# Kernel tuning notes

Hardware: AMD Instinct MI355X
Metric: run time of the kernel (lower is better)

The kernel has to match this reference:

```python
import jax, jax.numpy as jnp
import numpy as np

K_RATIO = 0.2
EPS = 1e-6


def setup_inputs() -> dict:
    key = jax.random.key(0)
    k1, k2 = jax.random.split(key)
    B, C, D, H, W = 2, 4, 128, 128, 128
    logits = jax.random.normal(k1, (B, C, D, H, W), dtype=jnp.float32)
    labels = jax.random.randint(k2, (B, D, H, W), 0, C)
    # one-hot target along channel axis 1, matching the tensor-path `target` arg
    target = jax.nn.one_hot(labels, C, axis=1, dtype=jnp.float32)
    return {"logits": logits, "target": target}


def reference(logits, target):
    B, C = logits.shape[0], logits.shape[1]

    # ---- Top-K cross entropy (ignore_index=-1 -> all voxels valid) ----
    y = jnp.argmax(target, axis=1)  # [B, D, H, W] int labels
    logp = jax.nn.log_softmax(logits, axis=1)
    # CE per voxel: -logp[b, y, d, h, w]
    ce = -jnp.take_along_axis(logp, y[:, None], axis=1)[:, 0]  # [B, D, H, W]
    ce_flat = ce.reshape(B, -1)  # [B, N]
    N = ce_flat.shape[1]
    k = max(1, int(N * K_RATIO))  # static: all voxels valid, k < N
    topk_vals, _ = jax.lax.top_k(ce_flat, k)  # [B, k]
    topk_loss = jnp.mean(jnp.mean(topk_vals, axis=1))

    # ---- Soft dice (no valid_mask in tensor path) ----
    p = jax.nn.softmax(logits, axis=1)  # [B, C, D, H, W]
    spatial = tuple(range(2, p.ndim))
    num = 2.0 * jnp.sum(p * target, axis=spatial)          # [B, C]
    den = jnp.sum(p + target, axis=spatial) + EPS          # [B, C]
    dice = 1.0 - num / den                                  # [B, C]
    if C > 1:
        dice = dice[:, 1:]  # drop background channel
    dice_loss = jnp.mean(dice)

    return topk_loss + 0.5 * dice_loss
```

## Files before the change

### kernel.cpp

```cpp
#include <hip/hip_runtime.h>
#include <stdint.h>

#define NVOX (1u << 21)
#define NB   2
#define KSEL 419430u
#define TPB  256
#define VPB  4096
#define BPB  ((int)(NVOX / VPB))
#define NBLK (NB * BPB)
#define NITER ((int)(VPB / (TPB * 4)))
#define NCOPY 64
#define NHC  16
#define NBINS 4096
#define SH   19
#define FIXS 262144.0f

typedef unsigned long long ull;

__device__ __forceinline__ float wred64(float v) {
#pragma unroll
  for (int o = 32; o > 0; o >>= 1) v += __shfl_down(v, o, 64);
  return v;
}

__global__ __launch_bounds__(TPB, 4) void k1_fused(
    const float* __restrict__ logits, const float* __restrict__ target,
    ull* __restrict__ hist,
    float* __restrict__ dice_acc )
{
  __shared__ ull hbin[NBINS];
  const int tid = threadIdx.x;
  for (int i = tid; i < NBINS; i += TPB) hbin[i] = 0ull;
  __syncthreads();

  const int blk = blockIdx.x;
  const int b = blk / BPB;
  const size_t v0 = (size_t)(blk % BPB) * VPB;
  const float* lg = logits + (size_t)b * 4 * NVOX + v0;
  const float* tg = target + (size_t)b * 4 * NVOX + v0;

  float sp[4] = {0.f,0.f,0.f,0.f}, nm[4] = {0.f,0.f,0.f,0.f}, ct[4] = {0.f,0.f,0.f,0.f};

  float4 La[4], Ta[4], Lb[4], Tb[4];
#pragma unroll
  for (int c = 0; c < 4; ++c) {
    La[c] = *(const float4*)(lg + (size_t)c * NVOX + tid * 4);
    Ta[c] = *(const float4*)(tg + (size_t)c * NVOX + tid * 4);
  }

#pragma unroll
  for (int it = 0; it < NITER; ++it) {
    if (it + 1 < NITER) {
      const int inx = (it + 1) * (TPB * 4) + tid * 4;
#pragma unroll
      for (int c = 0; c < 4; ++c) {
        Lb[c] = *(const float4*)(lg + (size_t)c * NVOX + inx);
        Tb[c] = *(const float4*)(tg + (size_t)c * NVOX + inx);
      }
    }
#pragma unroll
    for (int j = 0; j < 4; ++j) {
      float l[4], t[4];
#pragma unroll
      for (int c = 0; c < 4; ++c) {
        l[c] = ((const float*)&La[c])[j];
        t[c] = ((const float*)&Ta[c])[j];
      }
      float m = fmaxf(fmaxf(l[0], l[1]), fmaxf(l[2], l[3]));
      float e[4]; float s = 0.f;
#pragma unroll
      for (int c = 0; c < 4; ++c) { e[c] = __expf(l[c] - m); s += e[c]; }
      float inv = 1.f / s;
      float lse = __logf(s);
      float ly = l[0]*t[0] + l[1]*t[1] + l[2]*t[2] + l[3]*t[3];
      float cev = (m - ly) + lse;
      uint32_t idx = __float_as_uint(cev) >> SH;
      if (idx > NBINS - 1) idx = NBINS - 1;
      ull pk = (1ull << 40) | (ull)(cev * FIXS);
      atomicAdd(&hbin[idx], pk);
#pragma unroll
      for (int c = 0; c < 4; ++c) {
        float p = e[c] * inv;
        sp[c] += p;
        nm[c] += p * t[c];
        ct[c] += t[c];
      }
    }
    if (it + 1 < NITER) {
#pragma unroll
      for (int c = 0; c < 4; ++c) { La[c] = Lb[c]; Ta[c] = Tb[c]; }
    }
  }

#pragma unroll
  for (int c = 0; c < 4; ++c) { sp[c] = wred64(sp[c]); nm[c] = wred64(nm[c]); ct[c] = wred64(ct[c]); }
  if ((tid & 63) == 0) {
    float* dst = dice_acc + ((size_t)(blk & (NCOPY - 1)) * NB + b) * 12;
#pragma unroll
    for (int c = 0; c < 4; ++c) {
      atomicAdd(dst + c,     sp[c]);
      atomicAdd(dst + 4 + c, nm[c]);
      atomicAdd(dst + 8 + c, ct[c]);
    }
  }
  __syncthreads();
  const size_t hoff = ((size_t)b * NHC + (size_t)(blk & (NHC - 1))) * NBINS;
  ull* hdst = hist + hoff;
  for (int i = tid; i < NBINS; i += TPB) {
    ull v = hbin[i];
    if (v) atomicAdd(&hdst[i], v);
  }
}

__global__ __launch_bounds__(256) void k_reduce(
    const ull* __restrict__ hist,
    uint32_t* __restrict__ rcnt, float* __restrict__ rsum)
{
  const int b = blockIdx.x >> 3;
  const int base = (blockIdx.x & 7) * 512 + threadIdx.x * 2;
  uint32_t c0 = 0, c1 = 0;
  ull s0 = 0, s1 = 0;
  for (int copy = 0; copy < NHC; ++copy) {
    const ull* src = hist + ((size_t)b * NHC + copy) * NBINS + base;
    ull v0 = src[0], v1 = src[1];
    c0 += (uint32_t)(v0 >> 40); s0 += (v0 & 0xFFFFFFFFFFull);
    c1 += (uint32_t)(v1 >> 40); s1 += (v1 & 0xFFFFFFFFFFull);
  }
  rcnt[(size_t)b * NBINS + base]     = c0;
  rcnt[(size_t)b * NBINS + base + 1] = c1;
  rsum[(size_t)b * NBINS + base]     = (float)((double)s0 * (1.0 / 262144.0));
  rsum[(size_t)b * NBINS + base + 1] = (float)((double)s1 * (1.0 / 262144.0));
}

__global__ __launch_bounds__(256) void k_final(
    const uint32_t* __restrict__ rcnt, const float* __restrict__ rsum,
    const float* __restrict__ dice_acc, float* __restrict__ out)
{
  __shared__ uint32_t shc[NBINS];
  __shared__ uint32_t chunk[256];
  __shared__ uint32_t sbkt, srem;
  __shared__ float wpart[4];
  __shared__ float ts[NB];
  __shared__ float comp[24];
  const int tid = threadIdx.x;
  if (tid < 24) comp[tid] = 0.f;

  for (int b = 0; b < NB; ++b) {
    const uint32_t* rc = rcnt + (size_t)b * NBINS;
    const float*    rs = rsum + (size_t)b * NBINS;
    uint32_t s = 0;
#pragma unroll
    for (int q = 0; q < 4; ++q) {
      uint4 v = *(const uint4*)(rc + tid * 16 + q * 4);
      *(uint4*)&shc[tid * 16 + q * 4] = v;
      s += v.x + v.y + v.z + v.w;
    }
    chunk[tid] = s;
    __syncthreads();
    if (tid == 0) {
      uint32_t k = KSEL, cum = 0;
      int ci = 255;
      for (; ci > 0; --ci) {
        uint32_t c = chunk[ci];
        if (cum + c >= k) break;
        cum += c;
      }
      int bkt = ci * 16;
      for (int j = 15; j >= 0; --j) {
        uint32_t c = shc[ci * 16 + j];
        if (cum + c >= k) { bkt = ci * 16 + j; break; }
        cum += c;
      }
      sbkt = (uint32_t)bkt;
      srem = k - cum;
    }
    __syncthreads();
    const int bkt = (int)sbkt;
    float w = 0.f;
#pragma unroll
    for (int j = 0; j < 16; ++j) {
      int bin = tid * 16 + j;
      if (bin > bkt) w += rs[bin];
    }
    w = wred64(w);
    if ((tid & 63) == 0) wpart[tid >> 6] = w;
    __syncthreads();
    if (tid == 0) {
      float cnt_t = (float)shc[bkt];
      float sum_t = rs[bkt];
      float lo = __uint_as_float((uint32_t)bkt << SH);
      float hi = __uint_as_float((uint32_t)(bkt + 1) << SH);
      float width = hi - lo;
      float avg = sum_t / cnt_t;
      float frac = (float)srem / cnt_t;
      float est = avg + (1.f - frac) * 0.5f * width;
      ts[b] = wpart[0] + wpart[1] + wpart[2] + wpart[3] + (float)srem * est;
    }
    __syncthreads();
  }

  for (int x = tid; x < NCOPY * 24; x += 256)
    atomicAdd(&comp[x % 24], dice_acc[x]);
  __syncthreads();
  if (tid == 0) {
    float dl = 0.f;
#pragma unroll
    for (int b = 0; b < 2; ++b)
#pragma unroll
      for (int c = 1; c < 4; ++c) {
        float sp = comp[b * 12 + c];
        float nm = comp[b * 12 + 4 + c];
        float ct = comp[b * 12 + 8 + c];
        dl += 1.f - (2.f * nm) / (sp + ct + 1e-6f);
      }
    float topk = 0.5f * (ts[0] + ts[1]) / (float)KSEL;
    out[0] = topk + 0.5f * (dl / 6.f);
  }
}

extern "C" void kernel_launch(void* const* d_in, const int* in_sizes, int n_in,
                              void* d_out, int out_size, void* d_ws, size_t ws_size,
                              hipStream_t stream) {
  (void)in_sizes; (void)n_in; (void)out_size; (void)ws_size;
  const float* logits = (const float*)d_in[0];
  const float* target = (const float*)d_in[1];
  float* out = (float*)d_out;

  char* ws = (char*)d_ws;
  ull*      hist = (ull*)ws;
  float*    dice_acc = (float*)(hist + (size_t)NB * NHC * NBINS);
  uint32_t* rcnt = (uint32_t*)(dice_acc + (size_t)NCOPY * NB * 12);
  float*    rsum = (float*)(rcnt + (size_t)NB * NBINS);
  const size_t ZERO_BYTES = (size_t)((char*)rcnt - ws);

  hipMemsetAsync(ws, 0, ZERO_BYTES, stream);

  k1_fused<<<NBLK, TPB, 0, stream>>>(logits, target, hist, dice_acc);
  k_reduce<<<NB * 8, 256, 0, stream>>>(hist, rcnt, rsum);
  k_final<<<1, 256, 0, stream>>>(rcnt, rsum, dice_acc, out);
}
```

Before: 175.1 us.

## Stream inputs via async global-to-LDS loads with double-buffered tiles

The fused histogram/dice kernel stops using register-level float4 prefetching. Each wave now issues direct global_load_lds transfers for one channel of logits or target into a double-buffered shared tile. Threads then read one voxel's eight values from LDS, with explicit waitcnt and barriers coordinating the pipeline. Block size doubles to 512 threads covering 8192 voxels, which means fewer blocks but extra LDS (32KB of buffers plus the 32KB histogram) and two barriers per tile. The reduce loop also gets an unroll pragma.

Measured after the change: 187.7 us. 1.07x slower.

```diff
diff --git a/kernel.cpp b/kernel.cpp
--- a/kernel.cpp
+++ b/kernel.cpp
@@ -4,11 +4,12 @@
 #define NVOX (1u << 21)
 #define NB   2
 #define KSEL 419430u
-#define TPB  256
-#define VPB  4096
+#define TPB  512
+#define VPB  8192
 #define BPB  ((int)(NVOX / VPB))
 #define NBLK (NB * BPB)
-#define NITER ((int)(VPB / (TPB * 4)))
+#define TILE 512
+#define NTILE ((int)(VPB / TILE))
 #define NCOPY 64
 #define NHC  16
 #define NBINS 4096
@@ -23,11 +24,19 @@
   return v;
 }
 
+__device__ __forceinline__ void gload16(const float* g, float* l) {
+  __builtin_amdgcn_global_load_lds(
+      (__attribute__((address_space(1))) void*)g,
+      (__attribute__((address_space(3))) void*)l,
+      16, 0, 0);
+}
+
 __global__ __launch_bounds__(TPB, 4) void k1_fused(
     const float* __restrict__ logits, const float* __restrict__ target,
     ull* __restrict__ hist,
     float* __restrict__ dice_acc )
 {
+  __shared__ float sbuf[2][8 * TILE];
   __shared__ ull hbin[NBINS];
   const int tid = threadIdx.x;
   for (int i = tid; i < NBINS; i += TPB) hbin[i] = 0ull;
@@ -39,62 +48,65 @@
   const float* lg = logits + (size_t)b * 4 * NVOX + v0;
   const float* tg = target + (size_t)b * 4 * NVOX + v0;
 
+  const int w = tid >> 6, lane = tid & 63;
+  const float* sbase = (w < 4) ? (lg + (size_t)w * NVOX)
+                               : (tg + (size_t)(w - 4) * NVOX);
+
   float sp[4] = {0.f,0.f,0.f,0.f}, nm[4] = {0.f,0.f,0.f,0.f}, ct[4] = {0.f,0.f,0.f,0.f};
 
-  float4 La[4], Ta[4], Lb[4], Tb[4];
-#pragma unroll
-  for (int c = 0; c < 4; ++c) {
-    La[c] = *(const float4*)(lg + (size_t)c * NVOX + tid * 4);
-    Ta[c] = *(const float4*)(tg + (size_t)c * NVOX + tid * 4);
-  }
-
-#pragma unroll
-  for (int it = 0; it < NITER; ++it) {
-    if (it + 1 < NITER) {
-      const int inx = (it + 1) * (TPB * 4) + tid * 4;
-#pragma unroll
-      for (int c = 0; c < 4; ++c) {
-        Lb[c] = *(const float4*)(lg + (size_t)c * NVOX + inx);
-        Tb[c] = *(const float4*)(tg + (size_t)c * NVOX + inx);
-      }
-    }
-#pragma unroll
-    for (int j = 0; j < 4; ++j) {
-      float l[4], t[4];
-#pragma unroll
-      for (int c = 0; c < 4; ++c) {
-        l[c] = ((const float*)&La[c])[j];
-        t[c] = ((const float*)&Ta[c])[j];
-      }
-      float m = fmaxf(fmaxf(l[0], l[1]), fmaxf(l[2], l[3]));
-      float e[4]; float s = 0.f;
-#pragma unroll
-      for (int c = 0; c < 4; ++c) { e[c] = __expf(l[c] - m); s += e[c]; }
-      float inv = 1.f / s;
-      float lse = __logf(s);
-      float ly = l[0]*t[0] + l[1]*t[1] + l[2]*t[2] + l[3]*t[3];
-      float cev = (m - ly) + lse;
-      uint32_t idx = __float_as_uint(cev) >> SH;
-      if (idx > NBINS - 1) idx = NBINS - 1;
-      ull pk = (1ull << 40) | (ull)(cev * FIXS);
-      atomicAdd(&hbin[idx], pk);
-#pragma unroll
-      for (int c = 0; c < 4; ++c) {
-        float p = e[c] * inv;
-        sp[c] += p;
-        nm[c] += p * t[c];
-        ct[c] += t[c];
-      }
-    }
-    if (it + 1 < NITER) {
-#pragma unroll
-      for (int c = 0; c < 4; ++c) { La[c] = Lb[c]; Ta[c] = Tb[c]; }
-    }
-  }
+  auto ISSUE = [&](int t, int pb) {
+    const float* g0 = sbase + (size_t)t * TILE + lane * 4;
+    gload16(g0,       &sbuf[pb][w * TILE]);
+    gload16(g0 + 256, &sbuf[pb][w * TILE + 256]);
+  };
+
+  auto CONSUME = [&](int pb) {
+    float l[4], t[4];
+#pragma unroll
+    for (int c = 0; c < 4; ++c) {
+      l[c] = sbuf[pb][c * TILE + tid];
+      t[c] = sbuf[pb][(4 + c) * TILE + tid];
+    }
+    float m = fmaxf(fmaxf(l[0], l[1]), fmaxf(l[2], l[3]));
+    float e[4]; float s = 0.f;
+#pragma unroll
+    for (int c = 0; c < 4; ++c) { e[c] = __expf(l[c] - m); s += e[c]; }
+    float inv = 1.f / s;
+    float lse = __logf(s);
+    float ly = l[0]*t[0] + l[1]*t[1] + l[2]*t[2] + l[3]*t[3];
+    float cev = (m - ly) + lse;
+    uint32_t idx = __float_as_uint(cev) >> SH;
+    if (idx > NBINS - 1) idx = NBINS - 1;
+    ull pk = (1ull << 40) | (ull)(cev * FIXS);
+    atomicAdd(&hbin[idx], pk);
+#pragma unroll
+    for (int c = 0; c < 4; ++c) {
+      float p = e[c] * inv;
+      sp[c] += p;
+      nm[c] += p * t[c];
+      ct[c] += t[c];
+    }
+  };
+
+  ISSUE(0, 0);
+  ISSUE(1, 1);
+
+#pragma unroll 1
+  for (int t = 0; t < NTILE - 1; ++t) {
+    asm volatile("s_waitcnt vmcnt(2)" ::: "memory");
+    __builtin_amdgcn_s_barrier();
+    CONSUME(t & 1);
+    asm volatile("s_waitcnt lgkmcnt(0)" ::: "memory");
+    __builtin_amdgcn_s_barrier();
+    if (t + 2 < NTILE) ISSUE(t + 2, t & 1);
+  }
+  asm volatile("s_waitcnt vmcnt(0)" ::: "memory");
+  __builtin_amdgcn_s_barrier();
+  CONSUME((NTILE - 1) & 1);
 
 #pragma unroll
   for (int c = 0; c < 4; ++c) { sp[c] = wred64(sp[c]); nm[c] = wred64(nm[c]); ct[c] = wred64(ct[c]); }
-  if ((tid & 63) == 0) {
+  if (lane == 0) {
     float* dst = dice_acc + ((size_t)(blk & (NCOPY - 1)) * NB + b) * 12;
 #pragma unroll
     for (int c = 0; c < 4; ++c) {
@@ -120,6 +132,7 @@
   const int base = (blockIdx.x & 7) * 512 + threadIdx.x * 2;
   uint32_t c0 = 0, c1 = 0;
   ull s0 = 0, s1 = 0;
+#pragma unroll 4
   for (int copy = 0; copy < NHC; ++copy) {
     const ull* src = hist + ((size_t)b * NHC + copy) * NBINS + base;
     ull v0 = src[0], v1 = src[1];
```
